# Optimization experiments

Measured on AMD Instinct MI355X. Metric: run time of the kernel, lower is better.

## Reference

```python
import jax, jax.numpy as jnp
import numpy as np
import math

B, S, E, H = 4, 1024, 1024, 16
D = E // H
C = 1.0           # Poincare ball curvature
CS = math.sqrt(C)
EPS = 1e-7

def _sq(x):
    return jnp.sum(x * x, axis=-1, keepdims=True)

def expmap0(v):
    n = jnp.sqrt(jnp.clip(_sq(v), 1e-15))
    return jnp.tanh(CS * n) * v / (CS * n)

def logmap0(y):
    n = jnp.sqrt(jnp.clip(_sq(y), 1e-15))
    t = jnp.clip(CS * n, 0.0, 1.0 - 1e-6)
    return jnp.arctanh(t) * y / (CS * n)

def hlinear(x, z, r):
    # Poincare fully-connected layer (HNN++, Shimizu et al.), as in hypll HLinear
    lam = 2.0 / jnp.clip(1.0 - C * _sq(x), EPS)          # [..., 1] conformal factor
    zn = jnp.clip(jnp.linalg.norm(z, axis=0), 1e-15)     # [out]
    xz = x @ z                                           # [..., out]
    tcr = 2.0 * CS * r
    v = (2.0 * zn / CS) * jnp.arcsinh(CS * lam * xz / zn * jnp.cosh(tcr) - (lam - 1.0) * jnp.sinh(tcr))
    w = jnp.sinh(CS * v) / CS
    return w / (1.0 + jnp.sqrt(1.0 + C * jnp.sum(w * w, -1, keepdims=True)))

def _beta(a, b):
    return math.exp(math.lgamma(a) + math.lgamma(b) - math.lgamma(a + b))

def _forward(query, key, value, zq, bq, zk, bk, zv, bv):
    pq, pk, pv = hlinear(query, zq, bq), hlinear(key, zk, bk), hlinear(value, zv, bv)
    split = lambda x: x.reshape(B, S, H, D).transpose(0, 2, 1, 3)   # [B,H,S,D]
    q, k, v = split(pq), split(pk), split(pv)
    # attention_similarity: negative per-head pairwise Poincare distance (all heads vectorized)
    q2 = jnp.sum(q * q, -1)                              # [B,H,Sq]
    k2 = jnp.sum(k * k, -1)                              # [B,H,Sk]
    qk = jnp.einsum('bhqd,bhkd->bhqk', q, k)
    diff2 = jnp.clip(q2[..., :, None] + k2[..., None, :] - 2.0 * qk, 0.0)
    den = jnp.clip((1.0 - C * q2)[..., :, None] * (1.0 - C * k2)[..., None, :], EPS)
    dist = jnp.arccosh(jnp.clip(1.0 + 2.0 * C * diff2 / den, 1.0 + 1e-6)) / CS
    # attention_activation: softmax over keys
    w = jax.nn.softmax(-dist, axis=-1)                   # [B,H,Sq,Sk]
    # attention_midpoint: weighted gyromidpoint of values over keys
    lam = 2.0 / jnp.clip(1.0 - C * jnp.sum(v * v, -1), EPS)          # [B,H,Sk]
    num = jnp.einsum('bhqk,bhkd->bhqd', w * lam[..., None, :], v)
    dnm = jnp.clip(jnp.einsum('bhqk,bhk->bhq', jnp.abs(w), lam - 1.0), EPS)
    u = num / dnm[..., None]
    mid = u / (1.0 + jnp.sqrt(jnp.clip(1.0 - C * _sq(u), EPS)))      # (1/2) Mobius scalar mult
    # manifold.cat: beta-concatenation of heads (HNN++)
    scale = _beta(E / 2.0, 0.5) / _beta(D / 2.0, 0.5)
    tv = logmap0(mid) * scale                            # tangent at origin, [B,H,S,D]
    return expmap0(tv.transpose(0, 2, 1, 3).reshape(B, S, E))

def setup_inputs():
    key = jax.random.key(0)
    ks = jax.random.split(key, 9)
    mk = lambda k: expmap0(jax.random.normal(k, (B, S, E), jnp.float32) * (0.3 / math.sqrt(E)))
    zs = lambda k: jax.random.normal(k, (E, E), jnp.float32) / math.sqrt(E)
    bs = lambda k: jax.random.normal(k, (E,), jnp.float32) * 0.01
    return {"query": mk(ks[0]), "key": mk(ks[1]), "value": mk(ks[2]),
            "zq": zs(ks[3]), "bq": bs(ks[4]), "zk": zs(ks[5]), "bk": bs(ks[6]),
            "zv": zs(ks[7]), "bv": bs(ks[8])}

def reference(query, key, value, zq, bq, zk, bk, zv, bv):
    return _forward(query, key, value, zq, bq, zk, bk, zv, bv)
```

## Files before the change

kernel.cpp:

```cpp
#include <hip/hip_runtime.h>
#include <cmath>

#define EPSF 1e-7f

constexpr int B_ = 4, S_ = 1024, E_ = 1024, H_ = 16, D_ = 64;
constexpr int BS_ = B_ * S_;

typedef __attribute__((ext_vector_type(8))) short bf16x8;
typedef __attribute__((ext_vector_type(4))) float f32x4;

__device__ inline unsigned int fbits(float f) { union { float f; unsigned int u; } x; x.f = f; return x.u; }
__device__ inline float ubits(unsigned int u) { union { unsigned int u; float f; } x; x.u = u; return x.f; }

__device__ inline unsigned short f2bf(float f) {
  unsigned int u = fbits(f);
  unsigned int r = u + 0x7fffu + ((u >> 16) & 1u);
  return (unsigned short)(r >> 16);
}
__device__ inline float bf2f(unsigned short h) { return ubits(((unsigned int)h) << 16); }
__device__ inline float fastrcp(float x) { return __builtin_amdgcn_rcpf(x); }

__device__ __forceinline__ void async_ld16(const unsigned short* g, unsigned short* l) {
  __builtin_amdgcn_global_load_lds(
      (const __attribute__((address_space(1))) unsigned int*)g,
      (__attribute__((address_space(3))) unsigned int*)l, 16, 0, 0);
}

__global__ __launch_bounds__(256) void xsplit_kernel(
    const float* __restrict__ xq, const float* __restrict__ xk,
    const float* __restrict__ xv, unsigned short* __restrict__ Xbf,
    float* __restrict__ lamRow) {
  const int row = blockIdx.x;
  const float* x = (row < BS_) ? xq : (row < 2 * BS_ ? xk : xv);
  const int r = row & (BS_ - 1);
  const int tid = threadIdx.x;
  float4 v = ((const float4*)(x + (size_t)r * E_))[tid];
  float s = v.x * v.x + v.y * v.y + v.z * v.z + v.w * v.w;
  #pragma unroll
  for (int m = 1; m < 64; m <<= 1) s += __shfl_xor(s, m, 64);
  __shared__ float red[4];
  if ((tid & 63) == 0) red[tid >> 6] = s;
  __syncthreads();
  s = red[0] + red[1] + red[2] + red[3];
  uint2 p;
  p.x = (unsigned int)f2bf(v.x) | ((unsigned int)f2bf(v.y) << 16);
  p.y = (unsigned int)f2bf(v.z) | ((unsigned int)f2bf(v.w) << 16);
  ((uint2*)(Xbf + (size_t)row * E_))[tid] = p;
  if (tid == 0) lamRow[row] = 2.0f / fmaxf(1.0f - s, EPSF);
}

__global__ __launch_bounds__(256) void zsplit_kernel(
    const float* __restrict__ zq, const float* __restrict__ zk, const float* __restrict__ zv,
    unsigned short* __restrict__ BhiT, float* __restrict__ Zpart) {
  const int mat = blockIdx.z;
  const float* z = mat == 0 ? zq : (mat == 1 ? zk : zv);
  const int k0 = blockIdx.y * 64, n0 = blockIdx.x * 64;
  __shared__ float t[64][65];
  __shared__ float sred[64][4];
  const int tid = threadIdx.x;
  {
    int kr = tid >> 4, nc = (tid & 15) * 4;
    #pragma unroll
    for (int i = 0; i < 4; i++) {
      float4 vv = *(const float4*)(z + (size_t)(k0 + kr + i * 16) * E_ + n0 + nc);
      t[kr + i * 16][nc + 0] = vv.x;
      t[kr + i * 16][nc + 1] = vv.y;
      t[kr + i * 16][nc + 2] = vv.z;
      t[kr + i * 16][nc + 3] = vv.w;
    }
  }
  __syncthreads();
  int nr = tid >> 2, kc = (tid & 3) * 16;
  unsigned int ph[8];
  float ss = 0.f;
  #pragma unroll
  for (int p = 0; p < 8; p++) {
    float x0 = t[kc + 2 * p][nr], x1 = t[kc + 2 * p + 1][nr];
    ph[p] = (unsigned int)f2bf(x0) | ((unsigned int)f2bf(x1) << 16);
    ss += x0 * x0 + x1 * x1;
  }
  size_t off = (size_t)mat * E_ * E_ + (size_t)(n0 + nr) * E_ + k0 + kc;
  uint4* dh = (uint4*)(BhiT + off);
  dh[0] = make_uint4(ph[0], ph[1], ph[2], ph[3]);
  dh[1] = make_uint4(ph[4], ph[5], ph[6], ph[7]);
  sred[nr][tid & 3] = ss;
  __syncthreads();
  if (tid < 64) {
    float v = sred[tid][0] + sred[tid][1] + sred[tid][2] + sred[tid][3];
    Zpart[(size_t)(mat * 16 + blockIdx.y) * E_ + n0 + tid] = v;
  }
}

__global__ __launch_bounds__(256) void zstat_final_kernel(
    const float* __restrict__ Zpart,
    const float* __restrict__ bq, const float* __restrict__ bk, const float* __restrict__ bv,
    float* __restrict__ znA, float* __restrict__ chA, float* __restrict__ shA) {
  const int idx = blockIdx.x * 256 + threadIdx.x;
  const int mat = idx >> 10, col = idx & 1023;
  const float* bb = mat == 0 ? bq : (mat == 1 ? bk : bv);
  float s = 0.f;
  #pragma unroll
  for (int ky = 0; ky < 16; ky++)
    s += Zpart[(size_t)(mat * 16 + ky) * E_ + col];
  float n = fmaxf(sqrtf(s), 1e-15f);
  znA[idx] = n;
  float rb = bb[col];
  chA[idx] = coshf(2.f * rb);
  shA[idx] = sinhf(2.f * rb);
}

__global__ __launch_bounds__(256, 3) void hlinear_mfma_kernel(
    const unsigned short* __restrict__ Xbf,
    const unsigned short* __restrict__ BhiT,
    const float* __restrict__ lamRow, const float* __restrict__ znA,
    const float* __restrict__ chA, const float* __restrict__ shA,
    unsigned short* __restrict__ Wbf) {
  const int mat = blockIdx.z;
  const unsigned short* xa = Xbf + (size_t)mat * BS_ * E_;
  const unsigned short* bh = BhiT + (size_t)mat * E_ * E_;
  const int lid = blockIdx.y * 8 + blockIdx.x;
  const int sqi = lid >> 4, offb = lid & 15;
  const int m0 = ((sqi >> 1) * 4 + (offb & 3)) * 128;
  const int n0 = ((sqi & 1) * 4 + (offb >> 2)) * 128;

  __shared__ unsigned short LDSU[18432];
  unsigned short* As = LDSU;
  unsigned short* Bh = LDSU + 8192;

  const int tid = threadIdx.x;
  const int wid = tid >> 6, lane = tid & 63, quad = lane >> 4, l16 = lane & 15;
  const int wm = (wid >> 1) * 64, wn = (wid & 1) * 64;

  f32x4 acc[4][4];
  #pragma unroll
  for (int i = 0; i < 4; i++)
    #pragma unroll
    for (int j = 0; j < 4; j++) acc[i][j] = (f32x4){0.f, 0.f, 0.f, 0.f};

  const int lrow = lane >> 3;
  const int lcs = ((lane & 7) ^ lrow) * 8;
  const int xsw = (l16 & 7);

  for (int kt = 0; kt < E_ / 64; ++kt) {
    __syncthreads();
    const int kb = kt * 64 + lcs;
    #pragma unroll
    for (int c2 = 0; c2 < 4; c2++) {
      const int c = wid * 4 + c2;
      const int grow = c * 8 + lrow;
      async_ld16(xa + (size_t)(m0 + grow) * E_ + kb, As + c * 512);
      async_ld16(bh + (size_t)(n0 + grow) * E_ + kb, Bh + c * 512);
    }
    __syncthreads();
    #pragma unroll
    for (int h = 0; h < 2; h++) {
      bf16x8 a[4];
      #pragma unroll
      for (int mt = 0; mt < 4; mt++) {
        int row = wm + mt * 16 + l16;
        a[mt] = *(const bf16x8*)&As[row * 64 + (((h * 4 + quad) ^ xsw) * 8)];
      }
      #pragma unroll
      for (int nt = 0; nt < 4; nt++) {
        int row = wn + nt * 16 + l16;
        bf16x8 bhf = *(const bf16x8*)&Bh[row * 64 + (((h * 4 + quad) ^ xsw) * 8)];
        #pragma unroll
        for (int mt = 0; mt < 4; mt++)
          acc[mt][nt] = __builtin_amdgcn_mfma_f32_16x16x32_bf16(a[mt], bhf, acc[mt][nt], 0, 0, 0);
      }
    }
  }

  const float* lamP = lamRow + mat * BS_;
  float lamv[16];
  #pragma unroll
  for (int mt = 0; mt < 4; mt++)
    #pragma unroll
    for (int r = 0; r < 4; r++)
      lamv[mt * 4 + r] = lamP[m0 + wm + mt * 16 + quad * 4 + r];

  __syncthreads();
  unsigned short* epi = LDSU + wid * 4608;
  #pragma unroll
  for (int nt = 0; nt < 4; nt++) {
    int cg = n0 + wn + nt * 16 + l16;
    float zn = znA[mat * E_ + cg];
    float chzn = chA[mat * E_ + cg] / zn;
    float sh = shA[mat * E_ + cg];
    float tzn = 2.f * zn;
    #pragma unroll
    for (int mt = 0; mt < 4; mt++) {
      #pragma unroll
      for (int r = 0; r < 4; r++) {
        float lam = lamv[mt * 4 + r];
        float arg = fmaf(lam * acc[mt][nt][r], chzn, -(lam - 1.f) * sh);
        float sq2 = sqrtf(fmaf(arg, arg, 1.f));
        float v = tzn * __logf(arg + sq2);
        float ev = __expf(v);
        float w = 0.5f * (ev - fastrcp(ev));
        epi[(mt * 16 + quad * 4 + r) * 72 + nt * 16 + l16] = f2bf(w);
      }
    }
  }
  unsigned short* gout = Wbf + (size_t)mat * BS_ * E_ + (size_t)(m0 + wm) * E_ + n0 + wn;
  const int rrow = lane >> 3, seg = lane & 7;
  #pragma unroll
  for (int i = 0; i < 8; i++) {
    int row = i * 8 + rrow;
    uint4 val = *(const uint4*)&epi[row * 72 + seg * 8];
    *(uint4*)(gout + (size_t)row * E_ + seg * 8) = val;
  }
}

__global__ __launch_bounds__(256) void normalize_kernel(
    const unsigned short* __restrict__ Wbf, unsigned short* __restrict__ Pbf,
    float* __restrict__ HN) {
  const unsigned short* w = Wbf + (size_t)blockIdx.x * E_;
  int tid = threadIdx.x;
  uint2 wv = ((const uint2*)w)[tid];
  float w0 = bf2f((unsigned short)(wv.x & 0xFFFF));
  float w1 = bf2f((unsigned short)(wv.x >> 16));
  float w2 = bf2f((unsigned short)(wv.y & 0xFFFF));
  float w3 = bf2f((unsigned short)(wv.y >> 16));
  float s = w0 * w0 + w1 * w1 + w2 * w2 + w3 * w3;
  #pragma unroll
  for (int m = 1; m < 64; m <<= 1) s += __shfl_xor(s, m, 64);
  __shared__ float red[4];
  if ((tid & 63) == 0) red[tid >> 6] = s;
  __syncthreads();
  s = red[0] + red[1] + red[2] + red[3];
  float t = 1.f / (1.f + sqrtf(1.f + s));
  unsigned short p0 = f2bf(w0 * t), p1 = f2bf(w1 * t), p2 = f2bf(w2 * t), p3 = f2bf(w3 * t);
  uint2 pk;
  pk.x = (unsigned int)p0 | ((unsigned int)p1 << 16);
  pk.y = (unsigned int)p2 | ((unsigned int)p3 << 16);
  ((uint2*)(Pbf + (size_t)blockIdx.x * E_))[tid] = pk;
  float r0 = bf2f(p0), r1 = bf2f(p1), r2 = bf2f(p2), r3 = bf2f(p3);
  float hs = r0 * r0 + r1 * r1 + r2 * r2 + r3 * r3;
  hs += __shfl_xor(hs, 1, 64);
  hs += __shfl_xor(hs, 2, 64);
  hs += __shfl_xor(hs, 4, 64);
  hs += __shfl_xor(hs, 8, 64);
  if ((tid & 15) == 0) HN[(size_t)blockIdx.x * H_ + (tid >> 4)] = hs;
}

__global__ __launch_bounds__(256) void vtrans_kernel(
    const unsigned short* __restrict__ Pbf, const float* __restrict__ HN,
    unsigned short* __restrict__ KsG, unsigned short* __restrict__ VtG,
    unsigned short* __restrict__ lamMG, unsigned int* __restrict__ auxG) {
  const int st = blockIdx.x, h = blockIdx.y, b = blockIdx.z;
  const unsigned short* pk = Pbf + (size_t)BS_ * E_;
  const unsigned short* pv = Pbf + (size_t)2 * BS_ * E_;
  const float* hnk = HN + (size_t)BS_ * H_;
  const float* hnv = HN + (size_t)2 * BS_ * H_;
  __shared__ unsigned short T[64][72];
  __shared__ float lamS[64], cS[64];
  const int tid = threadIdx.x;
  const size_t bhS = (size_t)(b * H_ + h) * S_;
  {
    int lr = tid >> 2, lc = (tid & 3) * 16;
    const uint4* src = (const uint4*)(pv + (size_t)(b * S_ + st * 64 + lr) * E_ + h * 64 + lc);
    *(uint4*)&T[lr][lc] = src[0];
    *(uint4*)&T[lr][lc + 8] = src[1];
  }
  if (tid < 64) {
    float v2 = hnv[(size_t)(b * S_ + st * 64 + tid) * H_ + h];
    float lam = 2.f / fmaxf(1.f - v2, EPSF);
    lamS[tid] = lam;
    size_t sidx = bhS + st * 64 + tid;
    lamMG[sidx] = f2bf(lam - 1.f);
    float k2 = hnk[(size_t)(b * S_ + st * 64 + tid) * H_ + h];
    float rc = fastrcp(1.f - k2);
    cS[tid] = rc;
    auxG[sidx] = (unsigned int)f2bf(rc) | ((unsigned int)f2bf(rc * k2) << 16);
  }
  __syncthreads();
  {
    int d = tid >> 2, sc = (tid & 3) * 16;
    unsigned int o[8];
    #pragma unroll
    for (int i = 0; i < 8; i++) {
      int s0 = sc + 2 * i;
      float f0 = bf2f(T[s0][d]) * lamS[s0];
      float f1 = bf2f(T[s0 + 1][d]) * lamS[s0 + 1];
      o[i] = (unsigned int)f2bf(f0) | ((unsigned int)f2bf(f1) << 16);
    }
    unsigned short* dst = VtG + (bhS * 64) + (size_t)d * S_ + st * 64 + sc;
    ((uint4*)dst)[0] = make_uint4(o[0], o[1], o[2], o[3]);
    ((uint4*)dst)[1] = make_uint4(o[4], o[5], o[6], o[7]);
  }
  {
    int lr = tid >> 2, lc = (tid & 3) * 16;
    float c = cS[lr];
    const uint4* src = (const uint4*)(pk + (size_t)(b * S_ + st * 64 + lr) * E_ + h * 64 + lc);
    union { uint4 q; unsigned short s[8]; } i0, i1, o0, o1;
    i0.q = src[0]; i1.q = src[1];
    #pragma unroll
    for (int j = 0; j < 8; j++) {
      o0.s[j] = f2bf(bf2f(i0.s[j]) * c);
      o1.s[j] = f2bf(bf2f(i1.s[j]) * c);
    }
    unsigned short* dst = KsG + (bhS + st * 64 + lr) * 64 + lc;
    ((uint4*)dst)[0] = o0.q;
    ((uint4*)dst)[1] = o1.q;
  }
}

__global__ __launch_bounds__(512) void attention_kernel(
    const unsigned short* __restrict__ Pbf, const float* __restrict__ HN,
    const unsigned short* __restrict__ KsG, const unsigned short* __restrict__ VtG,
    const unsigned short* __restrict__ lamMG, const unsigned int* __restrict__ auxG,
    float* __restrict__ TV, float scale) {
  const int qt = blockIdx.x, h = blockIdx.y, b = blockIdx.z;
  const unsigned short* pq = Pbf;
  const float* hnq = HN;

  const int tid = threadIdx.x;
  const int wid = tid >> 6, lane = tid & 63;
  const int quad = lane >> 4, l16 = lane & 15;

  __shared__ __align__(16) unsigned short Kl[4096];
  __shared__ __align__(16) unsigned short Vl[4096];
  __shared__ __align__(16) unsigned short Pw[8][16][72];
  __shared__ __align__(16) unsigned short lamL[1024];
  __shared__ __align__(16) unsigned int auxL[1024];

  const size_t bhS = (size_t)(b * H_ + h) * S_;
  ((unsigned int*)lamL)[tid] = ((const unsigned int*)(lamMG + bhS))[tid];
  ((uint2*)auxL)[tid] = ((const uint2*)(auxG + bhS))[tid];

  const int qrow0 = qt * 128 + wid * 16;
  const size_t qgrow = ((size_t)(b * S_ + qrow0 + l16)) * E_ + h * 64;
  bf16x8 aq0r = *(const bf16x8*)(pq + qgrow + quad * 8);
  bf16x8 aq1r = *(const bf16x8*)(pq + qgrow + 32 + quad * 8);
  const float q2l = hnq[((size_t)(b * S_ + qrow0 + l16)) * H_ + h];
  const float al = 2.f * fastrcp(1.f - q2l);
  const float sc2 = -2.f * al;
  bf16x8 aq0, aq1;
  #pragma unroll
  for (int j = 0; j < 8; j++) {
    aq0[j] = (short)f2bf(bf2f((unsigned short)aq0r[j]) * sc2);
    aq1[j] = (short)f2bf(bf2f((unsigned short)aq1r[j]) * sc2);
  }
  const unsigned short ae0 = (quad == 0) ? f2bf(al * q2l) : 0;
  const unsigned short ae1 = (quad == 0) ? f2bf(al) : 0;
  const bf16x8 aex = (bf16x8){(short)ae0, (short)ae1, 0, 0, 0, 0, 0, 0};

  f32x4 accO[4];
  #pragma unroll
  for (int dt = 0; dt < 4; dt++) accO[dt] = (f32x4){0.f, 0.f, 0.f, 0.f};
  f32x4 accD = (f32x4){0.f, 0.f, 0.f, 0.f};

  const int lr = lane >> 3, cch = lane & 7;
  const int xsw = l16 & 7;
  const unsigned short* kbase = KsG + bhS * 64;
  const unsigned short* vbase = VtG + bhS * 64;

  for (int kt = 0; kt < S_ / 64; ++kt) {
    __syncthreads();
    {
      const int r = wid * 8 + lr;
      const int cc = ((cch ^ lr) * 8);
      async_ld16(kbase + (size_t)(kt * 64 + r) * 64 + cc, Kl + wid * 512);
      async_ld16(vbase + (size_t)r * S_ + kt * 64 + cc, Vl + wid * 512);
    }
    __syncthreads();

    #pragma unroll
    for (int nt = 0; nt < 4; nt++) {
      const int krow = nt * 16 + l16;
      bf16x8 bk0 = *(const bf16x8*)&Kl[krow * 64 + ((quad ^ xsw) * 8)];
      bf16x8 bk1 = *(const bf16x8*)&Kl[krow * 64 + (((4 + quad) ^ xsw) * 8)];
      unsigned int av = (quad == 0) ? auxL[kt * 64 + krow] : 0u;
      bf16x8 bex = (bf16x8){(short)(av & 0xFFFF), (short)(av >> 16), 0, 0, 0, 0, 0, 0};
      f32x4 z = (f32x4){0.f, 0.f, 0.f, 0.f};
      f32x4 st = __builtin_amdgcn_mfma_f32_16x16x32_bf16(aex, bex, z, 0, 0, 0);
      st = __builtin_amdgcn_mfma_f32_16x16x32_bf16(aq0, bk0, st, 0, 0, 0);
      st = __builtin_amdgcn_mfma_f32_16x16x32_bf16(aq1, bk1, st, 0, 0, 0);
      #pragma unroll
      for (int r2 = 0; r2 < 4; r2++) {
        float t = fmaxf(st[r2], 1e-6f);
        float A = 1.f + t;
        float w = A - sqrtf(fmaf(A, A, -1.f));
        Pw[wid][quad * 4 + r2][krow] = (unsigned short)(fbits(w) >> 16);
      }
    }
    bf16x8 ap0 = *(const bf16x8*)&Pw[wid][l16][quad * 8];
    bf16x8 ap1 = *(const bf16x8*)&Pw[wid][l16][32 + quad * 8];
    #pragma unroll
    for (int dt = 0; dt < 4; dt++) {
      const int drow = dt * 16 + l16;
      bf16x8 bv0 = *(const bf16x8*)&Vl[drow * 64 + ((quad ^ xsw) * 8)];
      bf16x8 bv1 = *(const bf16x8*)&Vl[drow * 64 + (((4 + quad) ^ xsw) * 8)];
      accO[dt] = __builtin_amdgcn_mfma_f32_16x16x32_bf16(ap0, bv0, accO[dt], 0, 0, 0);
      accO[dt] = __builtin_amdgcn_mfma_f32_16x16x32_bf16(ap1, bv1, accO[dt], 0, 0, 0);
    }
    bf16x8 bl0 = *(const bf16x8*)&lamL[kt * 64 + quad * 8];
    bf16x8 bl1 = *(const bf16x8*)&lamL[kt * 64 + 32 + quad * 8];
    accD = __builtin_amdgcn_mfma_f32_16x16x32_bf16(ap0, bl0, accD, 0, 0, 0);
    accD = __builtin_amdgcn_mfma_f32_16x16x32_bf16(ap1, bl1, accD, 0, 0, 0);
  }

  #pragma unroll
  for (int r2 = 0; r2 < 4; r2++) {
    float rdsum = 1.f / accD[r2];
    float uu[4];
    float su = 0.f;
    #pragma unroll
    for (int dt = 0; dt < 4; dt++) { uu[dt] = accO[dt][r2] * rdsum; su += uu[dt] * uu[dt]; }
    su += __shfl_xor(su, 1, 64);
    su += __shfl_xor(su, 2, 64);
    su += __shfl_xor(su, 4, 64);
    su += __shfl_xor(su, 8, 64);
    float g = 1.f / (1.f + sqrtf(fmaxf(1.f - su, EPSF)));
    float n2 = fmaxf(su * g * g, 1e-15f);
    float n = sqrtf(n2);
    float fac = atanhf(fminf(n, 1.f - 1e-6f)) / n * g * scale;
    size_t orow = ((size_t)(b * S_ + qrow0 + quad * 4 + r2)) * E_ + h * 64 + l16;
    #pragma unroll
    for (int dt = 0; dt < 4; dt++) TV[orow + dt * 16] = fac * uu[dt];
  }
}

__global__ __launch_bounds__(256) void expmap_kernel(float* __restrict__ TV) {
  float* w = TV + (size_t)blockIdx.x * E_;
  int tid = threadIdx.x;
  float4 v = ((float4*)w)[tid];
  float s = v.x * v.x + v.y * v.y + v.z * v.z + v.w * v.w;
  #pragma unroll
  for (int m = 1; m < 64; m <<= 1) s += __shfl_xor(s, m, 64);
  __shared__ float red[4];
  if ((tid & 63) == 0) red[tid >> 6] = s;
  __syncthreads();
  s = red[0] + red[1] + red[2] + red[3];
  float n = sqrtf(fmaxf(s, 1e-15f));
  float f = tanhf(n) / n;
  v.x *= f; v.y *= f; v.z *= f; v.w *= f;
  ((float4*)w)[tid] = v;
}

extern "C" void kernel_launch(void* const* d_in, const int* in_sizes, int n_in,
                              void* d_out, int out_size, void* d_ws, size_t ws_size,
                              hipStream_t stream) {
  (void)in_sizes; (void)n_in; (void)out_size; (void)ws_size;
  const float* q  = (const float*)d_in[0];
  const float* k  = (const float*)d_in[1];
  const float* v  = (const float*)d_in[2];
  const float* zq = (const float*)d_in[3];
  const float* bq = (const float*)d_in[4];
  const float* zk = (const float*)d_in[5];
  const float* bk = (const float*)d_in[6];
  const float* zv = (const float*)d_in[7];
  const float* bv = (const float*)d_in[8];

  unsigned short* Wbf = (unsigned short*)d_ws;
  unsigned short* Pbf = Wbf + (size_t)3 * BS_ * E_;
  unsigned short* BhiT = Pbf;
  unsigned short* Xbf = Pbf + (size_t)3 * BS_ * E_;
  float* HN           = (float*)(Xbf + (size_t)3 * BS_ * E_);
  float* lamRow       = HN + (size_t)3 * BS_ * H_;
  float* znA          = lamRow + 3 * BS_;
  float* chA          = znA + 3 * E_;
  float* shA          = chA + 3 * E_;
  float* Zpart        = shA + 3 * E_;
  unsigned short* VtG = (unsigned short*)(Zpart + 48 * E_);
  unsigned short* KsG = VtG + (size_t)B_ * H_ * 64 * S_;
  unsigned short* lamMG = KsG + (size_t)B_ * H_ * S_ * 64;
  unsigned int* auxG  = (unsigned int*)(lamMG + (size_t)B_ * H_ * S_);
  float* out          = (float*)d_out;

  double lb1 = lgamma(E_ / 2.0) + lgamma(0.5) - lgamma(E_ / 2.0 + 0.5);
  double lb2 = lgamma(D_ / 2.0) + lgamma(0.5) - lgamma(D_ / 2.0 + 0.5);
  float scale = (float)exp(lb1 - lb2);

  hipLaunchKernelGGL(xsplit_kernel, dim3(3 * BS_), dim3(256), 0, stream, q, k, v, Xbf, lamRow);
  hipLaunchKernelGGL(zsplit_kernel, dim3(16, 16, 3), dim3(256), 0, stream,
                     zq, zk, zv, BhiT, Zpart);
  hipLaunchKernelGGL(zstat_final_kernel, dim3(12), dim3(256), 0, stream,
                     Zpart, bq, bk, bv, znA, chA, shA);
  hipLaunchKernelGGL(hlinear_mfma_kernel, dim3(8, 32, 3), dim3(256), 0, stream,
                     Xbf, BhiT, lamRow, znA, chA, shA, Wbf);
  hipLaunchKernelGGL(normalize_kernel, dim3(3 * BS_), dim3(256), 0, stream, Wbf, Pbf, HN);
  hipLaunchKernelGGL(vtrans_kernel, dim3(16, 16, 4), dim3(256), 0, stream,
                     Pbf, HN, KsG, VtG, lamMG, auxG);
  hipLaunchKernelGGL(attention_kernel, dim3(8, 16, 4), dim3(512), 0, stream,
                     Pbf, HN, KsG, VtG, lamMG, auxG, out, scale);
  hipLaunchKernelGGL(expmap_kernel, dim3(BS_), dim3(256), 0, stream, out);
}
```

Baseline: 244.9 us.

## Double-buffer K/V tiles and keep attention weights in registers via permlane swaps

K and V tiles now go into two LDS buffers: the next tile is prefetched asynchronously while the current one is processed, and there is one barrier per iteration instead of two. The score MFMA operands are swapped so the result comes out transposed. The weights are then packed to bf16 with v_cvt_pk_bf16_f32 and rearranged across lanes with permlane32/16 swaps into the A-operand layout, which removes the per-wave LDS round-trip through the Pw buffer. Rounding changes from truncation to round-to-nearest. LDS use grows for the extra K/V buffers, and correctness depends on the permlane shuffle producing exactly the expected layout.

```diff
diff --git a/kernel.cpp b/kernel.cpp
--- a/kernel.cpp
+++ b/kernel.cpp
@@ -24,6 +24,18 @@
   __builtin_amdgcn_global_load_lds(
       (const __attribute__((address_space(1))) unsigned int*)g,
       (__attribute__((address_space(3))) unsigned int*)l, 16, 0, 0);
+}
+
+__device__ __forceinline__ unsigned int cvt_pk_bf16(float lo, float hi) {
+  unsigned int r;
+  asm("v_cvt_pk_bf16_f32 %0, %1, %2" : "=v"(r) : "v"(lo), "v"(hi));
+  return r;
+}
+__device__ __forceinline__ void permlane32_swap(unsigned int &a, unsigned int &b) {
+  asm("v_permlane32_swap_b32 %0, %1" : "+v"(a), "+v"(b));
+}
+__device__ __forceinline__ void permlane16_swap(unsigned int &a, unsigned int &b) {
+  asm("v_permlane16_swap_b32 %0, %1" : "+v"(a), "+v"(b));
 }
 
 __global__ __launch_bounds__(256) void xsplit_kernel(
@@ -319,9 +331,8 @@
   const int wid = tid >> 6, lane = tid & 63;
   const int quad = lane >> 4, l16 = lane & 15;
 
-  __shared__ __align__(16) unsigned short Kl[4096];
-  __shared__ __align__(16) unsigned short Vl[4096];
-  __shared__ __align__(16) unsigned short Pw[8][16][72];
+  __shared__ __align__(16) unsigned short Kl[2][4096];
+  __shared__ __align__(16) unsigned short Vl[2][4096];
   __shared__ __align__(16) unsigned short lamL[1024];
   __shared__ __align__(16) unsigned int auxL[1024];
 
@@ -355,43 +366,60 @@
   const int xsw = l16 & 7;
   const unsigned short* kbase = KsG + bhS * 64;
   const unsigned short* vbase = VtG + bhS * 64;
+  const int srow = wid * 8 + lr;
+  const int scc = ((cch ^ lr) * 8);
+
+  async_ld16(kbase + (size_t)srow * 64 + scc, &Kl[0][wid * 512]);
+  async_ld16(vbase + (size_t)srow * S_ + scc, &Vl[0][wid * 512]);
+  __syncthreads();
 
   for (int kt = 0; kt < S_ / 64; ++kt) {
-    __syncthreads();
-    {
-      const int r = wid * 8 + lr;
-      const int cc = ((cch ^ lr) * 8);
-      async_ld16(kbase + (size_t)(kt * 64 + r) * 64 + cc, Kl + wid * 512);
-      async_ld16(vbase + (size_t)r * S_ + kt * 64 + cc, Vl + wid * 512);
-    }
-    __syncthreads();
-
+    const int buf = kt & 1;
+    if (kt + 1 < S_ / 64) {
+      async_ld16(kbase + (size_t)((kt + 1) * 64 + srow) * 64 + scc, &Kl[buf ^ 1][wid * 512]);
+      async_ld16(vbase + (size_t)srow * S_ + (kt + 1) * 64 + scc, &Vl[buf ^ 1][wid * 512]);
+    }
+
+    unsigned int Wp[4][2];
     #pragma unroll
     for (int nt = 0; nt < 4; nt++) {
       const int krow = nt * 16 + l16;
-      bf16x8 bk0 = *(const bf16x8*)&Kl[krow * 64 + ((quad ^ xsw) * 8)];
-      bf16x8 bk1 = *(const bf16x8*)&Kl[krow * 64 + (((4 + quad) ^ xsw) * 8)];
+      bf16x8 bk0 = *(const bf16x8*)&Kl[buf][krow * 64 + ((quad ^ xsw) * 8)];
+      bf16x8 bk1 = *(const bf16x8*)&Kl[buf][krow * 64 + (((4 + quad) ^ xsw) * 8)];
       unsigned int av = (quad == 0) ? auxL[kt * 64 + krow] : 0u;
       bf16x8 bex = (bf16x8){(short)(av & 0xFFFF), (short)(av >> 16), 0, 0, 0, 0, 0, 0};
       f32x4 z = (f32x4){0.f, 0.f, 0.f, 0.f};
-      f32x4 st = __builtin_amdgcn_mfma_f32_16x16x32_bf16(aex, bex, z, 0, 0, 0);
-      st = __builtin_amdgcn_mfma_f32_16x16x32_bf16(aq0, bk0, st, 0, 0, 0);
-      st = __builtin_amdgcn_mfma_f32_16x16x32_bf16(aq1, bk1, st, 0, 0, 0);
+      f32x4 st = __builtin_amdgcn_mfma_f32_16x16x32_bf16(bex, aex, z, 0, 0, 0);
+      st = __builtin_amdgcn_mfma_f32_16x16x32_bf16(bk0, aq0, st, 0, 0, 0);
+      st = __builtin_amdgcn_mfma_f32_16x16x32_bf16(bk1, aq1, st, 0, 0, 0);
+      float w[4];
       #pragma unroll
       for (int r2 = 0; r2 < 4; r2++) {
         float t = fmaxf(st[r2], 1e-6f);
         float A = 1.f + t;
-        float w = A - sqrtf(fmaf(A, A, -1.f));
-        Pw[wid][quad * 4 + r2][krow] = (unsigned short)(fbits(w) >> 16);
+        w[r2] = A - sqrtf(fmaf(A, A, -1.f));
       }
-    }
-    bf16x8 ap0 = *(const bf16x8*)&Pw[wid][l16][quad * 8];
-    bf16x8 ap1 = *(const bf16x8*)&Pw[wid][l16][32 + quad * 8];
+      Wp[nt][0] = cvt_pk_bf16(w[0], w[1]);
+      Wp[nt][1] = cvt_pk_bf16(w[2], w[3]);
+    }
+    unsigned int x00 = Wp[0][0], y00 = Wp[1][0];
+    permlane32_swap(x00, y00); permlane16_swap(x00, y00);
+    unsigned int x01 = Wp[0][1], y01 = Wp[1][1];
+    permlane32_swap(x01, y01); permlane16_swap(x01, y01);
+    unsigned int x10 = Wp[2][0], y10 = Wp[3][0];
+    permlane32_swap(x10, y10); permlane16_swap(x10, y10);
+    unsigned int x11 = Wp[2][1], y11 = Wp[3][1];
+    permlane32_swap(x11, y11); permlane16_swap(x11, y11);
+    union { unsigned int u[4]; bf16x8 v; } ap0u, ap1u;
+    ap0u.u[0] = x00; ap0u.u[1] = x01; ap0u.u[2] = y00; ap0u.u[3] = y01;
+    ap1u.u[0] = x10; ap1u.u[1] = x11; ap1u.u[2] = y10; ap1u.u[3] = y11;
+    const bf16x8 ap0 = ap0u.v, ap1 = ap1u.v;
+
     #pragma unroll
     for (int dt = 0; dt < 4; dt++) {
       const int drow = dt * 16 + l16;
-      bf16x8 bv0 = *(const bf16x8*)&Vl[drow * 64 + ((quad ^ xsw) * 8)];
-      bf16x8 bv1 = *(const bf16x8*)&Vl[drow * 64 + (((4 + quad) ^ xsw) * 8)];
+      bf16x8 bv0 = *(const bf16x8*)&Vl[buf][drow * 64 + ((quad ^ xsw) * 8)];
+      bf16x8 bv1 = *(const bf16x8*)&Vl[buf][drow * 64 + (((4 + quad) ^ xsw) * 8)];
       accO[dt] = __builtin_amdgcn_mfma_f32_16x16x32_bf16(ap0, bv0, accO[dt], 0, 0, 0);
       accO[dt] = __builtin_amdgcn_mfma_f32_16x16x32_bf16(ap1, bv1, accO[dt], 0, 0, 0);
     }
@@ -399,6 +427,8 @@
     bf16x8 bl1 = *(const bf16x8*)&lamL[kt * 64 + 32 + quad * 8];
     accD = __builtin_amdgcn_mfma_f32_16x16x32_bf16(ap0, bl0, accD, 0, 0, 0);
     accD = __builtin_amdgcn_mfma_f32_16x16x32_bf16(ap1, bl1, accD, 0, 0, 0);
+
+    __syncthreads();
   }
 
   #pragma unroll
```

After: 252.4 us. 3.1% more time.
